# Performance work log

Measured on AMD Instinct MI355X. Metric: run time of the kernel, lower is better.

Reference implementation:

```python
import jax, jax.numpy as jnp
import numpy as np

H = 32
DECAY = 0.9


def setup_inputs() -> dict:
    key = jax.random.key(0)
    ks = jax.random.split(key, 6)
    B, T, D = 8, 4096, 1024
    x = jax.random.normal(ks[0], (B, T, D), dtype=jnp.float32)
    s = 1.0 / np.sqrt(D)
    Wv = jax.random.normal(ks[1], (D, D), dtype=jnp.float32) * s
    bv = jax.random.normal(ks[2], (D,), dtype=jnp.float32) * s
    Wo = jax.random.normal(ks[3], (D, D), dtype=jnp.float32) * s
    bo = jax.random.normal(ks[4], (D,), dtype=jnp.float32) * s
    w = jnp.asarray(DECAY ** np.arange(H), dtype=jnp.float32)
    decay_w = w / jnp.sum(w)
    return {"x": x, "Wv": Wv, "bv": bv, "Wo": Wo, "bo": bo, "decay_w": decay_w}


def reference(x, Wv, bv, Wo, bo, decay_w):
    # x: [B, T, D]. Original pads H zeros at front and unfolds windows of size H
    # with stride 1, producing T+1 windows: window t covers x[t-H .. t-1].
    # value_proj is linear and applied to every window copy, so it commutes with
    # the fixed-weight sum: attended = (sum_i w_i * x_window_i) @ Wv^T + bv*sum(w).
    B, T, D = x.shape
    Hlen = decay_w.shape[0]
    x_pad = jnp.pad(x, ((0, 0), (Hlen, 0), (0, 0)))  # [B, T+H, D]
    # Depthwise 1D conv over time with the (shared) decay kernel.
    kernel = jnp.broadcast_to(decay_w[:, None, None], (Hlen, 1, D))  # [W, I=1, O=D]
    s = jax.lax.conv_general_dilated(
        x_pad, kernel, window_strides=(1,), padding="VALID",
        dimension_numbers=("NWC", "WIO", "NWC"), feature_group_count=D,
    )  # [B, T+1, D]
    attended = s @ Wv.T + bv * jnp.sum(decay_w)
    return attended @ Wo.T + bo  # [B, T+1, D]
```

## Files before the change

### kernel.cpp

```cpp
#include <hip/hip_runtime.h>
#include <stdint.h>

#define D_DIM 1024
#define T_DIM 4096
#define B_DIM 8
#define M_REAL (B_DIM * (T_DIM + 1))
#define M_MAIN 32768
#define NWG 512

typedef short short8 __attribute__((ext_vector_type(8)));
typedef float floatx4 __attribute__((ext_vector_type(4)));

typedef const __attribute__((address_space(1))) void* gptr_t;
typedef __attribute__((address_space(3))) void* lptr_t;

__device__ __forceinline__ ushort f2bf(float f) {
  union { float f; uint32_t u; } v; v.f = f;
  uint32_t r = v.u + 0x7FFF + ((v.u >> 16) & 1);
  return (ushort)(r >> 16);
}
__device__ __forceinline__ float bf2f(ushort b) {
  union { uint32_t u; float f; } v; v.u = ((uint32_t)b) << 16; return v.f;
}

#define BARRIER()  asm volatile("s_barrier" ::: "memory")
#define WAIT_VM8() asm volatile("s_waitcnt vmcnt(8)" ::: "memory")
#define WAIT_VM0() asm volatile("s_waitcnt vmcnt(0)" ::: "memory")
#define WAIT_LGKM0() do { asm volatile("s_waitcnt lgkmcnt(0)" ::: "memory"); \
                          __builtin_amdgcn_sched_barrier(0); } while (0)
#define WAIT_LGKM4() do { asm volatile("s_waitcnt lgkmcnt(4)" ::: "memory"); \
                          __builtin_amdgcn_sched_barrier(0); } while (0)
#define WAIT_LGKM8() do { asm volatile("s_waitcnt lgkmcnt(8)" ::: "memory"); \
                          __builtin_amdgcn_sched_barrier(0); } while (0)
#define SP1() __builtin_amdgcn_s_setprio(1)
#define SP0() __builtin_amdgcn_s_setprio(0)

__global__ __launch_bounds__(512, 2) void gemm256_kernel(
    const ushort* __restrict__ A, const ushort* __restrict__ Bm,
    float* __restrict__ C, const float* __restrict__ bias)
{
  __shared__ char smem[131072];
  const int tid  = threadIdx.x;
  const int wave = tid >> 6;
  const int lane = tid & 63;
  const int wm = wave >> 2, wn = wave & 3;
  const int l15 = lane & 15, lhi = lane >> 4;
  const int rsw = (l15 & 7) << 4;

  const int bid = blockIdx.x;
  const int wg  = (bid & 7) * 64 + (bid >> 3);
  const int n0 = (wg & 3) * 256;
  const int m0 = (wg >> 2) * 256;

  const int rowc = tid >> 3;
  const int ksw  = ((tid ^ ((tid >> 3) & 7)) & 7) * 8;

  const ushort* Asrc[2][2]; const ushort* Bsrc[2][2];
#pragma unroll
  for (int h = 0; h < 2; ++h)
#pragma unroll
    for (int j = 0; j < 2; ++j) {
      Asrc[h][j] = A  + (size_t)(m0 + h * 128 + rowc + j * 64) * D_DIM + ksw;
      Bsrc[h][j] = Bm + (size_t)(n0 + h * 128 + rowc + j * 64) * D_DIM + ksw;
    }

#define STAGE_A(H, U, BUF) do { \
  __builtin_amdgcn_global_load_lds((gptr_t)(Asrc[H][0] + (U) * 64), \
      (lptr_t)(smem + ((BUF) * 2 + (H)) * 16384 + wave * 1024), 16, 0, 0); \
  __builtin_amdgcn_global_load_lds((gptr_t)(Asrc[H][1] + (U) * 64), \
      (lptr_t)(smem + ((BUF) * 2 + (H)) * 16384 + 8192 + wave * 1024), 16, 0, 0); \
} while (0)
#define STAGE_B(H, U, BUF) do { \
  __builtin_amdgcn_global_load_lds((gptr_t)(Bsrc[H][0] + (U) * 64), \
      (lptr_t)(smem + 65536 + ((BUF) * 2 + (H)) * 16384 + wave * 1024), 16, 0, 0); \
  __builtin_amdgcn_global_load_lds((gptr_t)(Bsrc[H][1] + (U) * 64), \
      (lptr_t)(smem + 65536 + ((BUF) * 2 + (H)) * 16384 + 8192 + wave * 1024), 16, 0, 0); \
} while (0)

  short8 a0[4], a1[4];
  short8 bfr[2][4];
  floatx4 acc[8][4] = {};

#define LDA(DST, MH, KK, BUF) do { \
  const char* _ab = smem + ((BUF) * 2 + wm) * 16384; \
  _Pragma("unroll") \
  for (int mp = 0; mp < 4; ++mp) { \
    int o = (((MH) * 64 + mp * 16 + l15) * 128 + (KK) * 64 + lhi * 16) ^ rsw; \
    DST[mp] = *(const short8*)(_ab + o); \
  } } while (0)
#define LDB(KK, BUF) do { \
  const char* _bb = smem + 65536 + ((BUF) * 2 + (wn >> 1)) * 16384; \
  _Pragma("unroll") \
  for (int n = 0; n < 4; ++n) { \
    int o = (((wn & 1) * 64 + n * 16 + l15) * 128 + (KK) * 64 + lhi * 16) ^ rsw; \
    bfr[KK][n] = *(const short8*)(_bb + o); \
  } } while (0)

#define MFMA16(MH, KK, FR) do { \
  _Pragma("unroll") \
  for (int mp = 0; mp < 4; ++mp) \
    _Pragma("unroll") \
    for (int n = 0; n < 4; ++n) \
      acc[(MH) * 4 + mp][n] = __builtin_amdgcn_mfma_f32_16x16x32_bf16( \
          FR[mp], bfr[KK][n], acc[(MH) * 4 + mp][n], 0, 0, 0); \
} while (0)

  STAGE_A(0, 0, 0); STAGE_A(1, 0, 0);
  STAGE_B(0, 0, 0); STAGE_B(1, 0, 0);
  STAGE_B(0, 1, 1); STAGE_B(1, 1, 1);

  for (int u = 0; u < 15; ++u) {
    const int buf = u & 1, nbuf = buf ^ 1;
    STAGE_A(0, u + 1, nbuf); STAGE_A(1, u + 1, nbuf);
    WAIT_VM8();
    BARRIER();
    LDB(0, buf); LDA(a0, 0, 0, buf); LDB(1, buf); LDA(a1, 0, 1, buf);
    WAIT_LGKM8();
    SP1(); MFMA16(0, 0, a0); SP0();
    WAIT_LGKM0();
    SP1(); MFMA16(0, 1, a1); SP0();
    BARRIER();
    if (u < 14) { STAGE_B(0, u + 2, buf); STAGE_B(1, u + 2, buf); }
    LDA(a0, 1, 0, buf); LDA(a1, 1, 1, buf);
    WAIT_LGKM4();
    SP1(); MFMA16(1, 0, a0); SP0();
    WAIT_LGKM0();
    SP1(); MFMA16(1, 1, a1); SP0();
    BARRIER();
  }
  {
    WAIT_VM0();
    BARRIER();
    LDB(0, 1); LDA(a0, 0, 0, 1); LDB(1, 1); LDA(a1, 0, 1, 1);
    WAIT_LGKM8(); SP1(); MFMA16(0, 0, a0); SP0();
    WAIT_LGKM0(); SP1(); MFMA16(0, 1, a1); SP0();
    LDA(a0, 1, 0, 1); LDA(a1, 1, 1, 1);
    WAIT_LGKM4(); SP1(); MFMA16(1, 0, a0); SP0();
    WAIT_LGKM0(); SP1(); MFMA16(1, 1, a1); SP0();
  }

#pragma unroll
  for (int m = 0; m < 8; ++m)
#pragma unroll
    for (int n = 0; n < 4; ++n) {
      const int gn = n0 + wn * 64 + n * 16 + l15;
      const float bia = bias[gn];
#pragma unroll
      for (int j = 0; j < 4; ++j) {
        const int gm = m0 + wm * 128 + m * 16 + lhi * 4 + j;
        C[(size_t)gm * D_DIM + gn] = acc[m][n][j] + bia;
      }
    }
#undef STAGE_A
#undef STAGE_B
#undef LDA
#undef LDB
#undef MFMA16
}

__global__ __launch_bounds__(256) void tail_gemv_kernel(
    const ushort* __restrict__ S, const ushort* __restrict__ Wf,
    const float* __restrict__ cvec, float* __restrict__ out)
{
  const int wavei = threadIdx.x >> 6, lane = threadIdx.x & 63;
  const int c = blockIdx.x * 4 + wavei;
  float acc[8] = {};
  for (int i = 0; i < 16; ++i) {
    const int k = i * 64 + lane;
    const float wv = bf2f(Wf[(size_t)c * D_DIM + k]);
#pragma unroll
    for (int r = 0; r < 8; ++r)
      acc[r] += wv * bf2f(S[(size_t)(M_MAIN + r) * D_DIM + k]);
  }
#pragma unroll
  for (int r = 0; r < 8; ++r) {
#pragma unroll
    for (int off = 32; off; off >>= 1) acc[r] += __shfl_xor(acc[r], off, 64);
  }
  if (lane == 0) {
    const float bia = cvec[c];
#pragma unroll
    for (int r = 0; r < 8; ++r)
      out[(size_t)(M_MAIN + r) * D_DIM + c] = acc[r] + bia;
  }
}

__global__ __launch_bounds__(256) void gemm_bt_kernel(
    const ushort* __restrict__ A, const ushort* __restrict__ Bm,
    ushort* __restrict__ Cb, int K, int N)
{
  __shared__ ushort As[128][64];
  __shared__ ushort Bs[128][64];
  const int tid  = threadIdx.x;
  const int wave = tid >> 6;
  const int lane = tid & 63;
  const int wm = wave >> 1, wn = wave & 1;
  const int n0 = blockIdx.x * 128, m0 = blockIdx.y * 128;
  const int l15 = lane & 15, lhi = lane >> 4;

  floatx4 acc[4][4] = {};

  const int srow = tid >> 3;
  const int sk8  = (tid & 7) * 8;
  const ushort* Ab = A  + (size_t)(m0 + srow) * K + sk8;
  const ushort* Bb = Bm + (size_t)(n0 + srow) * K + sk8;

  for (int k0 = 0; k0 < K; k0 += 64) {
#pragma unroll
    for (int q = 0; q < 4; ++q)
      __builtin_amdgcn_global_load_lds((gptr_t)(Ab + k0 + (size_t)q * 32 * K),
          (lptr_t)((char*)&As[0][0] + (q * 256 + wave * 64) * 16), 16, 0, 0);
#pragma unroll
    for (int q = 0; q < 4; ++q)
      __builtin_amdgcn_global_load_lds((gptr_t)(Bb + k0 + (size_t)q * 32 * K),
          (lptr_t)((char*)&Bs[0][0] + (q * 256 + wave * 64) * 16), 16, 0, 0);
    __syncthreads();

#pragma unroll
    for (int kk = 0; kk < 2; ++kk) {
      short8 af[4], bfrg[4];
#pragma unroll
      for (int i = 0; i < 4; ++i) {
        af[i]   = *(const short8*)(&As[wm * 64 + i * 16 + l15][kk * 32 + lhi * 8]);
        bfrg[i] = *(const short8*)(&Bs[wn * 64 + i * 16 + l15][kk * 32 + lhi * 8]);
      }
#pragma unroll
      for (int mi = 0; mi < 4; ++mi)
#pragma unroll
        for (int ni = 0; ni < 4; ++ni)
          acc[mi][ni] = __builtin_amdgcn_mfma_f32_16x16x32_bf16(
              af[mi], bfrg[ni], acc[mi][ni], 0, 0, 0);
    }
    __syncthreads();
  }

#pragma unroll
  for (int mi = 0; mi < 4; ++mi)
#pragma unroll
    for (int ni = 0; ni < 4; ++ni) {
      const int gn = n0 + wn * 64 + ni * 16 + l15;
#pragma unroll
      for (int j = 0; j < 4; ++j) {
        const int gm = m0 + wm * 64 + mi * 16 + lhi * 4 + j;
        Cb[(size_t)gm * N + gn] = f2bf(acc[mi][ni][j]);
      }
    }
}

#define CTCH 128
__global__ __launch_bounds__(256) void conv_kernel(
    const float* __restrict__ x, const float* __restrict__ dw,
    ushort* __restrict__ S)
{
  const int b   = blockIdx.y;
  const int col = blockIdx.z * 256 + threadIdx.x;
  const int t0  = blockIdx.x * CTCH;

  float w[32];
#pragma unroll
  for (int i = 0; i < 32; ++i) w[i] = dw[i];
  const float rinv = w[0] / w[1];
  const float w31  = w[31];
  const float c0   = -w[0] * rinv;

  const float* xb = x + (size_t)b * T_DIM * D_DIM + col;
  ushort*      Sb = S + (size_t)b * (T_DIM + 1) * D_DIM + col;

  float prev[32], cur[32];
  float s;
  if (blockIdx.x == 0) {
#pragma unroll
    for (int i = 0; i < 32; ++i) prev[i] = 0.f;
    s = 0.f;
    Sb[0] = f2bf(0.f);
  } else {
#pragma unroll
    for (int i = 0; i < 32; ++i) prev[i] = xb[(size_t)(t0 - 32 + i) * D_DIM];
    s = 0.f;
#pragma unroll
    for (int i = 0; i < 32; ++i) s = __builtin_fmaf(w[i], prev[i], s);
  }

#pragma unroll 1
  for (int g = 0; g < 4; g += 2) {
#pragma unroll
    for (int i = 0; i < 32; ++i) cur[i] = xb[(size_t)(t0 + g * 32 + i) * D_DIM];
#pragma unroll
    for (int j = 0; j < 32; ++j) {
      s = __builtin_fmaf(s, rinv, __builtin_fmaf(prev[j], c0, w31 * cur[j]));
      Sb[(size_t)(t0 + g * 32 + 1 + j) * D_DIM] = f2bf(s);
    }
    s = 0.f;
#pragma unroll
    for (int i = 0; i < 32; ++i) s = __builtin_fmaf(w[i], cur[i], s);
#pragma unroll
    for (int i = 0; i < 32; ++i) prev[i] = xb[(size_t)(t0 + (g + 1) * 32 + i) * D_DIM];
#pragma unroll
    for (int j = 0; j < 32; ++j) {
      s = __builtin_fmaf(s, rinv, __builtin_fmaf(cur[j], c0, w31 * prev[j]));
      Sb[(size_t)(t0 + (g + 1) * 32 + 1 + j) * D_DIM] = f2bf(s);
    }
    s = 0.f;
#pragma unroll
    for (int i = 0; i < 32; ++i) s = __builtin_fmaf(w[i], prev[i], s);
  }
}

__global__ void convert_wo_kernel(const float* __restrict__ Wo, ushort* __restrict__ WoB) {
  const int i = blockIdx.x * 256 + threadIdx.x;
  const float4 v = ((const float4*)Wo)[i];
  ushort4 o = make_ushort4(f2bf(v.x), f2bf(v.y), f2bf(v.z), f2bf(v.w));
  *(ushort4*)(WoB + (size_t)i * 4) = o;
}

__global__ void transpose_wv_kernel(const float* __restrict__ Wv, ushort* __restrict__ WvT) {
  __shared__ float tile[32][33];
  const int tx = threadIdx.x;
  const int ty = threadIdx.y;
  const int c0 = blockIdx.x * 32;
  const int r0 = blockIdx.y * 32;
#pragma unroll
  for (int j = 0; j < 4; ++j)
    tile[ty + j * 8][tx] = Wv[(size_t)(r0 + ty + j * 8) * D_DIM + c0 + tx];
  __syncthreads();
#pragma unroll
  for (int j = 0; j < 4; ++j)
    WvT[(size_t)(c0 + ty + j * 8) * D_DIM + r0 + tx] = f2bf(tile[tx][ty + j * 8]);
}

__global__ void bias_kernel(const float* __restrict__ Wo, const float* __restrict__ bv,
                            const float* __restrict__ bo, const float* __restrict__ dw,
                            float* __restrict__ cvec) {
  const int j    = blockIdx.x * 4 + (threadIdx.x >> 6);
  const int lane = threadIdx.x & 63;
  float sumw = 0.f;
#pragma unroll
  for (int i = 0; i < 32; ++i) sumw += dw[i];
  float s = 0.f;
  for (int k = lane; k < D_DIM; k += 64) s += Wo[(size_t)j * D_DIM + k] * bv[k];
#pragma unroll
  for (int off = 32; off; off >>= 1) s += __shfl_xor(s, off, 64);
  if (lane == 0) cvec[j] = sumw * s + bo[j];
}

extern "C" void kernel_launch(void* const* d_in, const int* in_sizes, int n_in,
                              void* d_out, int out_size, void* d_ws, size_t ws_size,
                              hipStream_t stream) {
  const float* x  = (const float*)d_in[0];
  const float* Wv = (const float*)d_in[1];
  const float* bv = (const float*)d_in[2];
  const float* Wo = (const float*)d_in[3];
  const float* bo = (const float*)d_in[4];
  const float* dw = (const float*)d_in[5];
  float* out = (float*)d_out;

  char* ws = (char*)d_ws;
  ushort* S      = (ushort*)ws;
  ushort* WoB    = (ushort*)(ws + (size_t)M_REAL * D_DIM * 2);
  ushort* WvT    = WoB + (size_t)D_DIM * D_DIM;
  ushort* Wfused = WvT + (size_t)D_DIM * D_DIM;
  float*  cvec   = (float*)(Wfused + (size_t)D_DIM * D_DIM);

  convert_wo_kernel<<<dim3(D_DIM * D_DIM / 1024), dim3(256), 0, stream>>>(Wo, WoB);
  transpose_wv_kernel<<<dim3(32, 32), dim3(32, 8), 0, stream>>>(Wv, WvT);
  bias_kernel<<<dim3(256), dim3(256), 0, stream>>>(Wo, bv, bo, dw, cvec);

  gemm_bt_kernel<<<dim3(8, 8), dim3(256), 0, stream>>>(
      WoB, WvT, Wfused, D_DIM, D_DIM);

  conv_kernel<<<dim3(T_DIM / CTCH, B_DIM, 4), dim3(256), 0, stream>>>(x, dw, S);

  gemm256_kernel<<<dim3(NWG), dim3(512), 0, stream>>>(S, Wfused, out, cvec);
  tail_gemv_kernel<<<dim3(256), dim3(256), 0, stream>>>(S, Wfused, cvec, out);
}
```

Measured before the change: 166.4 us.

## Restructure GEMM main loop into 8-wave ping-pong quadrant schedule

Reorganizes the 256x256 bf16 GEMM K-loop into four MFMA quadrants (M-half by N-half) over full K=64 fragments. Global-to-LDS staging of A and B halves is interleaved between quadrants, with more barriers and a vmcnt(6) wait, and the peeled final iteration is removed. Launch bounds drop the min-2-blocks-per-CU hint, freeing registers for the doubled A fragment sets. This aims at better overlap of LDS reads, global loads and MFMA work. The extra barriers may add synchronization stalls, and occupancy may fall.

```diff
diff --git a/kernel.cpp b/kernel.cpp
--- a/kernel.cpp
+++ b/kernel.cpp
@@ -24,18 +24,15 @@
 }
 
 #define BARRIER()  asm volatile("s_barrier" ::: "memory")
-#define WAIT_VM8() asm volatile("s_waitcnt vmcnt(8)" ::: "memory")
+#define WAIT_VM6() asm volatile("s_waitcnt vmcnt(6)" ::: "memory")
 #define WAIT_VM0() asm volatile("s_waitcnt vmcnt(0)" ::: "memory")
+#define WAIT_LGKM8_PRE() asm volatile("s_waitcnt lgkmcnt(8)" ::: "memory")
 #define WAIT_LGKM0() do { asm volatile("s_waitcnt lgkmcnt(0)" ::: "memory"); \
-                          __builtin_amdgcn_sched_barrier(0); } while (0)
-#define WAIT_LGKM4() do { asm volatile("s_waitcnt lgkmcnt(4)" ::: "memory"); \
-                          __builtin_amdgcn_sched_barrier(0); } while (0)
-#define WAIT_LGKM8() do { asm volatile("s_waitcnt lgkmcnt(8)" ::: "memory"); \
                           __builtin_amdgcn_sched_barrier(0); } while (0)
 #define SP1() __builtin_amdgcn_s_setprio(1)
 #define SP0() __builtin_amdgcn_s_setprio(0)
 
-__global__ __launch_bounds__(512, 2) void gemm256_kernel(
+__global__ __launch_bounds__(512) void gemm256_kernel(
     const ushort* __restrict__ A, const ushort* __restrict__ Bm,
     float* __restrict__ C, const float* __restrict__ bias)
 {
@@ -77,66 +74,74 @@
       (lptr_t)(smem + 65536 + ((BUF) * 2 + (H)) * 16384 + 8192 + wave * 1024), 16, 0, 0); \
 } while (0)
 
-  short8 a0[4], a1[4];
-  short8 bfr[2][4];
+  short8 am0[2][4], am1[2][4];
+  short8 b[2][4];
   floatx4 acc[8][4] = {};
 
-#define LDA(DST, MH, KK, BUF) do { \
+#define LDA_Q(DST, MQ, BUF) do { \
   const char* _ab = smem + ((BUF) * 2 + wm) * 16384; \
   _Pragma("unroll") \
-  for (int mp = 0; mp < 4; ++mp) { \
-    int o = (((MH) * 64 + mp * 16 + l15) * 128 + (KK) * 64 + lhi * 16) ^ rsw; \
-    DST[mp] = *(const short8*)(_ab + o); \
-  } } while (0)
-#define LDB(KK, BUF) do { \
+  for (int kk = 0; kk < 2; ++kk) \
+    _Pragma("unroll") \
+    for (int mp = 0; mp < 4; ++mp) { \
+      int o = (((MQ) * 64 + mp * 16 + l15) * 128 + kk * 64 + lhi * 16) ^ rsw; \
+      DST[kk][mp] = *(const short8*)(_ab + o); \
+    } } while (0)
+#define LDB_ALL(BUF) do { \
   const char* _bb = smem + 65536 + ((BUF) * 2 + (wn >> 1)) * 16384; \
   _Pragma("unroll") \
-  for (int n = 0; n < 4; ++n) { \
-    int o = (((wn & 1) * 64 + n * 16 + l15) * 128 + (KK) * 64 + lhi * 16) ^ rsw; \
-    bfr[KK][n] = *(const short8*)(_bb + o); \
-  } } while (0)
-
-#define MFMA16(MH, KK, FR) do { \
+  for (int kk = 0; kk < 2; ++kk) \
+    _Pragma("unroll") \
+    for (int nf = 0; nf < 4; ++nf) { \
+      int o = (((wn & 1) * 64 + nf * 16 + l15) * 128 + kk * 64 + lhi * 16) ^ rsw; \
+      b[kk][nf] = *(const short8*)(_bb + o); \
+    } } while (0)
+
+#define MFMA_Q(MQ, NQ, ASET) do { \
+  SP1(); \
   _Pragma("unroll") \
-  for (int mp = 0; mp < 4; ++mp) \
+  for (int kk = 0; kk < 2; ++kk) \
     _Pragma("unroll") \
-    for (int n = 0; n < 4; ++n) \
-      acc[(MH) * 4 + mp][n] = __builtin_amdgcn_mfma_f32_16x16x32_bf16( \
-          FR[mp], bfr[KK][n], acc[(MH) * 4 + mp][n], 0, 0, 0); \
+    for (int mp = 0; mp < 4; ++mp) \
+      _Pragma("unroll") \
+      for (int nj = 0; nj < 2; ++nj) \
+        acc[(MQ) * 4 + mp][(NQ) * 2 + nj] = \
+            __builtin_amdgcn_mfma_f32_16x16x32_bf16( \
+                ASET[kk][mp], b[kk][(NQ) * 2 + nj], \
+                acc[(MQ) * 4 + mp][(NQ) * 2 + nj], 0, 0, 0); \
+  SP0(); \
 } while (0)
 
-  STAGE_A(0, 0, 0); STAGE_A(1, 0, 0);
-  STAGE_B(0, 0, 0); STAGE_B(1, 0, 0);
-  STAGE_B(0, 1, 1); STAGE_B(1, 1, 1);
-
-  for (int u = 0; u < 15; ++u) {
+  STAGE_B(0, 0, 0); STAGE_B(1, 0, 0); STAGE_A(0, 0, 0); STAGE_A(1, 0, 0);
+  STAGE_B(0, 1, 1); STAGE_B(1, 1, 1); STAGE_A(0, 1, 1);
+  WAIT_VM6();
+  BARRIER();
+
+  for (int u = 0; u < 16; ++u) {
     const int buf = u & 1, nbuf = buf ^ 1;
-    STAGE_A(0, u + 1, nbuf); STAGE_A(1, u + 1, nbuf);
-    WAIT_VM8();
-    BARRIER();
-    LDB(0, buf); LDA(a0, 0, 0, buf); LDB(1, buf); LDA(a1, 0, 1, buf);
-    WAIT_LGKM8();
-    SP1(); MFMA16(0, 0, a0); SP0();
+    LDB_ALL(buf); LDA_Q(am0, 0, buf);
+    if (u < 15) STAGE_A(1, u + 1, nbuf);
+    WAIT_LGKM8_PRE();
+    BARRIER();
     WAIT_LGKM0();
-    SP1(); MFMA16(0, 1, a1); SP0();
-    BARRIER();
-    if (u < 14) { STAGE_B(0, u + 2, buf); STAGE_B(1, u + 2, buf); }
-    LDA(a0, 1, 0, buf); LDA(a1, 1, 1, buf);
-    WAIT_LGKM4();
-    SP1(); MFMA16(1, 0, a0); SP0();
+    MFMA_Q(0, 0, am0);
+    BARRIER();
+    LDA_Q(am1, 1, buf);
+    if (u < 14) STAGE_B(0, u + 2, buf);
+    BARRIER();
     WAIT_LGKM0();
-    SP1(); MFMA16(1, 1, a1); SP0();
-    BARRIER();
-  }
-  {
-    WAIT_VM0();
-    BARRIER();
-    LDB(0, 1); LDA(a0, 0, 0, 1); LDB(1, 1); LDA(a1, 0, 1, 1);
-    WAIT_LGKM8(); SP1(); MFMA16(0, 0, a0); SP0();
-    WAIT_LGKM0(); SP1(); MFMA16(0, 1, a1); SP0();
-    LDA(a0, 1, 0, 1); LDA(a1, 1, 1, 1);
-    WAIT_LGKM4(); SP1(); MFMA16(1, 0, a0); SP0();
-    WAIT_LGKM0(); SP1(); MFMA16(1, 1, a1); SP0();
+    MFMA_Q(1, 0, am1);
+    BARRIER();
+    if (u < 14) STAGE_B(1, u + 2, buf);
+    BARRIER();
+    MFMA_Q(0, 1, am0);
+    BARRIER();
+    if (u < 14) STAGE_A(0, u + 2, buf);
+    if (u <= 13) { WAIT_VM6(); }
+    else if (u == 14) { WAIT_VM0(); }
+    BARRIER();
+    MFMA_Q(1, 1, am1);
+    BARRIER();
   }
 
 #pragma unroll
@@ -153,9 +158,9 @@
     }
 #undef STAGE_A
 #undef STAGE_B
-#undef LDA
-#undef LDB
-#undef MFMA16
+#undef LDA_Q
+#undef LDB_ALL
+#undef MFMA_Q
 }
 
 __global__ __launch_bounds__(256) void tail_gemv_kernel(
```

New measurement: 192.5 us. +15.7%, slower.

## Replace pipelined 256x256 GEMM with simpler 128x128 tile kernel

Applied to the files above, without the earlier changes.

Swaps the hand-scheduled double-buffered 256x256 tile GEMM (512 threads, priority hints, fine-grained waits) for a 128x128 tile kernel with 256 threads and a single LDS buffer per operand. More, smaller workgroups may raise occupancy and spread work more evenly. In exchange it loses load/compute overlap, halves per-tile data reuse, and relies on barriers to order asynchronous LDS loads.

```diff
diff --git a/kernel.cpp b/kernel.cpp
--- a/kernel.cpp
+++ b/kernel.cpp
@@ -6,7 +6,6 @@
 #define B_DIM 8
 #define M_REAL (B_DIM * (T_DIM + 1))
 #define M_MAIN 32768
-#define NWG 512
 
 typedef short short8 __attribute__((ext_vector_type(8)));
 typedef float floatx4 __attribute__((ext_vector_type(4)));
@@ -23,139 +22,74 @@
   union { uint32_t u; float f; } v; v.u = ((uint32_t)b) << 16; return v.f;
 }
 
-#define BARRIER()  asm volatile("s_barrier" ::: "memory")
-#define WAIT_VM8() asm volatile("s_waitcnt vmcnt(8)" ::: "memory")
-#define WAIT_VM0() asm volatile("s_waitcnt vmcnt(0)" ::: "memory")
-#define WAIT_LGKM0() do { asm volatile("s_waitcnt lgkmcnt(0)" ::: "memory"); \
-                          __builtin_amdgcn_sched_barrier(0); } while (0)
-#define WAIT_LGKM4() do { asm volatile("s_waitcnt lgkmcnt(4)" ::: "memory"); \
-                          __builtin_amdgcn_sched_barrier(0); } while (0)
-#define WAIT_LGKM8() do { asm volatile("s_waitcnt lgkmcnt(8)" ::: "memory"); \
-                          __builtin_amdgcn_sched_barrier(0); } while (0)
-#define SP1() __builtin_amdgcn_s_setprio(1)
-#define SP0() __builtin_amdgcn_s_setprio(0)
-
-__global__ __launch_bounds__(512, 2) void gemm256_kernel(
+__global__ __launch_bounds__(256) void gemm128_kernel(
     const ushort* __restrict__ A, const ushort* __restrict__ Bm,
     float* __restrict__ C, const float* __restrict__ bias)
 {
-  __shared__ char smem[131072];
+  __shared__ ushort As[128][64];
+  __shared__ ushort Bs[128][64];
   const int tid  = threadIdx.x;
   const int wave = tid >> 6;
   const int lane = tid & 63;
-  const int wm = wave >> 2, wn = wave & 3;
+  const int wm = wave >> 1, wn = wave & 1;
   const int l15 = lane & 15, lhi = lane >> 4;
   const int rsw = (l15 & 7) << 4;
 
   const int bid = blockIdx.x;
-  const int wg  = (bid & 7) * 64 + (bid >> 3);
-  const int n0 = (wg & 3) * 256;
-  const int m0 = (wg >> 2) * 256;
-
-  const int rowc = tid >> 3;
-  const int ksw  = ((tid ^ ((tid >> 3) & 7)) & 7) * 8;
-
-  const ushort* Asrc[2][2]; const ushort* Bsrc[2][2];
-#pragma unroll
-  for (int h = 0; h < 2; ++h)
-#pragma unroll
-    for (int j = 0; j < 2; ++j) {
-      Asrc[h][j] = A  + (size_t)(m0 + h * 128 + rowc + j * 64) * D_DIM + ksw;
-      Bsrc[h][j] = Bm + (size_t)(n0 + h * 128 + rowc + j * 64) * D_DIM + ksw;
-    }
-
-#define STAGE_A(H, U, BUF) do { \
-  __builtin_amdgcn_global_load_lds((gptr_t)(Asrc[H][0] + (U) * 64), \
-      (lptr_t)(smem + ((BUF) * 2 + (H)) * 16384 + wave * 1024), 16, 0, 0); \
-  __builtin_amdgcn_global_load_lds((gptr_t)(Asrc[H][1] + (U) * 64), \
-      (lptr_t)(smem + ((BUF) * 2 + (H)) * 16384 + 8192 + wave * 1024), 16, 0, 0); \
-} while (0)
-#define STAGE_B(H, U, BUF) do { \
-  __builtin_amdgcn_global_load_lds((gptr_t)(Bsrc[H][0] + (U) * 64), \
-      (lptr_t)(smem + 65536 + ((BUF) * 2 + (H)) * 16384 + wave * 1024), 16, 0, 0); \
-  __builtin_amdgcn_global_load_lds((gptr_t)(Bsrc[H][1] + (U) * 64), \
-      (lptr_t)(smem + 65536 + ((BUF) * 2 + (H)) * 16384 + 8192 + wave * 1024), 16, 0, 0); \
-} while (0)
-
-  short8 a0[4], a1[4];
-  short8 bfr[2][4];
-  floatx4 acc[8][4] = {};
-
-#define LDA(DST, MH, KK, BUF) do { \
-  const char* _ab = smem + ((BUF) * 2 + wm) * 16384; \
-  _Pragma("unroll") \
-  for (int mp = 0; mp < 4; ++mp) { \
-    int o = (((MH) * 64 + mp * 16 + l15) * 128 + (KK) * 64 + lhi * 16) ^ rsw; \
-    DST[mp] = *(const short8*)(_ab + o); \
-  } } while (0)
-#define LDB(KK, BUF) do { \
-  const char* _bb = smem + 65536 + ((BUF) * 2 + (wn >> 1)) * 16384; \
-  _Pragma("unroll") \
-  for (int n = 0; n < 4; ++n) { \
-    int o = (((wn & 1) * 64 + n * 16 + l15) * 128 + (KK) * 64 + lhi * 16) ^ rsw; \
-    bfr[KK][n] = *(const short8*)(_bb + o); \
-  } } while (0)
-
-#define MFMA16(MH, KK, FR) do { \
-  _Pragma("unroll") \
-  for (int mp = 0; mp < 4; ++mp) \
-    _Pragma("unroll") \
-    for (int n = 0; n < 4; ++n) \
-      acc[(MH) * 4 + mp][n] = __builtin_amdgcn_mfma_f32_16x16x32_bf16( \
-          FR[mp], bfr[KK][n], acc[(MH) * 4 + mp][n], 0, 0, 0); \
-} while (0)
-
-  STAGE_A(0, 0, 0); STAGE_A(1, 0, 0);
-  STAGE_B(0, 0, 0); STAGE_B(1, 0, 0);
-  STAGE_B(0, 1, 1); STAGE_B(1, 1, 1);
-
-  for (int u = 0; u < 15; ++u) {
-    const int buf = u & 1, nbuf = buf ^ 1;
-    STAGE_A(0, u + 1, nbuf); STAGE_A(1, u + 1, nbuf);
-    WAIT_VM8();
-    BARRIER();
-    LDB(0, buf); LDA(a0, 0, 0, buf); LDB(1, buf); LDA(a1, 0, 1, buf);
-    WAIT_LGKM8();
-    SP1(); MFMA16(0, 0, a0); SP0();
-    WAIT_LGKM0();
-    SP1(); MFMA16(0, 1, a1); SP0();
-    BARRIER();
-    if (u < 14) { STAGE_B(0, u + 2, buf); STAGE_B(1, u + 2, buf); }
-    LDA(a0, 1, 0, buf); LDA(a1, 1, 1, buf);
-    WAIT_LGKM4();
-    SP1(); MFMA16(1, 0, a0); SP0();
-    WAIT_LGKM0();
-    SP1(); MFMA16(1, 1, a1); SP0();
-    BARRIER();
-  }
-  {
-    WAIT_VM0();
-    BARRIER();
-    LDB(0, 1); LDA(a0, 0, 0, 1); LDB(1, 1); LDA(a1, 0, 1, 1);
-    WAIT_LGKM8(); SP1(); MFMA16(0, 0, a0); SP0();
-    WAIT_LGKM0(); SP1(); MFMA16(0, 1, a1); SP0();
-    LDA(a0, 1, 0, 1); LDA(a1, 1, 1, 1);
-    WAIT_LGKM4(); SP1(); MFMA16(1, 0, a0); SP0();
-    WAIT_LGKM0(); SP1(); MFMA16(1, 1, a1); SP0();
-  }
-
-#pragma unroll
-  for (int m = 0; m < 8; ++m)
-#pragma unroll
-    for (int n = 0; n < 4; ++n) {
-      const int gn = n0 + wn * 64 + n * 16 + l15;
+  const int wg  = (bid & 7) * 256 + (bid >> 3);
+  const int n0 = (wg & 7) * 128;
+  const int m0 = (wg >> 3) * 128;
+
+  const int srow = tid >> 3;
+  const int ksw  = ((tid & 7) ^ (srow & 7)) * 8;
+  const ushort* Ab = A  + (size_t)(m0 + srow) * D_DIM + ksw;
+  const ushort* Bb = Bm + (size_t)(n0 + srow) * D_DIM + ksw;
+
+  floatx4 acc[4][4] = {};
+
+  for (int k0 = 0; k0 < D_DIM; k0 += 64) {
+#pragma unroll
+    for (int q = 0; q < 4; ++q)
+      __builtin_amdgcn_global_load_lds((gptr_t)(Ab + k0 + (size_t)q * 32 * D_DIM),
+          (lptr_t)((char*)&As[0][0] + (q * 256 + wave * 64) * 16), 16, 0, 0);
+#pragma unroll
+    for (int q = 0; q < 4; ++q)
+      __builtin_amdgcn_global_load_lds((gptr_t)(Bb + k0 + (size_t)q * 32 * D_DIM),
+          (lptr_t)((char*)&Bs[0][0] + (q * 256 + wave * 64) * 16), 16, 0, 0);
+    __syncthreads();
+
+#pragma unroll
+    for (int kk = 0; kk < 2; ++kk) {
+      short8 af[4], bfrg[4];
+#pragma unroll
+      for (int i = 0; i < 4; ++i) {
+        const int oa = ((wm * 64 + i * 16 + l15) * 128 + kk * 64 + lhi * 16) ^ rsw;
+        const int ob = ((wn * 64 + i * 16 + l15) * 128 + kk * 64 + lhi * 16) ^ rsw;
+        af[i]   = *(const short8*)((const char*)&As[0][0] + oa);
+        bfrg[i] = *(const short8*)((const char*)&Bs[0][0] + ob);
+      }
+#pragma unroll
+      for (int mi = 0; mi < 4; ++mi)
+#pragma unroll
+        for (int ni = 0; ni < 4; ++ni)
+          acc[mi][ni] = __builtin_amdgcn_mfma_f32_16x16x32_bf16(
+              af[mi], bfrg[ni], acc[mi][ni], 0, 0, 0);
+    }
+    __syncthreads();
+  }
+
+#pragma unroll
+  for (int mi = 0; mi < 4; ++mi)
+#pragma unroll
+    for (int ni = 0; ni < 4; ++ni) {
+      const int gn = n0 + wn * 64 + ni * 16 + l15;
       const float bia = bias[gn];
 #pragma unroll
       for (int j = 0; j < 4; ++j) {
-        const int gm = m0 + wm * 128 + m * 16 + lhi * 4 + j;
-        C[(size_t)gm * D_DIM + gn] = acc[m][n][j] + bia;
+        const int gm = m0 + wm * 64 + mi * 16 + lhi * 4 + j;
+        C[(size_t)gm * D_DIM + gn] = acc[mi][ni][j] + bia;
       }
     }
-#undef STAGE_A
-#undef STAGE_B
-#undef LDA
-#undef LDB
-#undef MFMA16
 }
 
 __global__ __launch_bounds__(256) void tail_gemv_kernel(
@@ -370,6 +304,6 @@
 
   conv_kernel<<<dim3(T_DIM / CTCH, B_DIM, 4), dim3(256), 0, stream>>>(x, dw, S);
 
-  gemm256_kernel<<<dim3(NWG), dim3(512), 0, stream>>>(S, Wfused, out, cvec);
+  gemm128_kernel<<<dim3(2048), dim3(256), 0, stream>>>(S, Wfused, out, cvec);
   tail_gemv_kernel<<<dim3(256), dim3(256), 0, stream>>>(S, Wfused, cvec, out);
 }
```

After: 169.1 us. No clear change (+1.6%).
